# Performance work log

Measured on AMD Instinct MI355X. Metric: run time of the kernel, lower is better.

Reference implementation:

```python
import jax, jax.numpy as jnp
import numpy as np

N = 100_000
E = 1_600_000
D_IN, D_HID, D_OUT = 512, 256, 256


def setup_inputs() -> dict:
    key = jax.random.key(0)
    ks = jax.random.split(key, 10)
    x = jax.random.normal(ks[0], (N, D_IN), dtype=jnp.float32)
    edge_index = jax.random.randint(ks[1], (2, E), 0, N, dtype=jnp.int64)
    edge_weight = jax.random.uniform(ks[2], (E,), dtype=jnp.float32)
    # Glorot-ish init for the per-layer linear weights (PyG GCNConv: Linear w/o bias, bias added after aggregation)
    W1 = jax.random.normal(ks[3], (D_IN, D_HID), dtype=jnp.float32) * (1.0 / np.sqrt(D_IN))
    b1 = jnp.zeros((D_HID,), dtype=jnp.float32)
    W2 = jax.random.normal(ks[4], (D_HID, D_HID), dtype=jnp.float32) * (1.0 / np.sqrt(D_HID))
    b2 = jnp.zeros((D_HID,), dtype=jnp.float32)
    W3 = jax.random.normal(ks[5], (D_HID, D_OUT), dtype=jnp.float32) * (1.0 / np.sqrt(D_HID))
    b3 = jnp.zeros((D_OUT,), dtype=jnp.float32)
    return {"x": x, "edge_index": edge_index, "edge_weight": edge_weight,
            "W1": W1, "b1": b1, "W2": W2, "b2": b2, "W3": W3, "b3": b3}


def gcn_layer(h_in, W, b, row, col, ew, n):
    # PyG GCNConv with normalize=True, add_self_loops=True (fill value 1.0), aggr='add':
    # h = X W; deg[i] = sum of incoming edge weights (incl. self loop);
    # norm_e = deg^-1/2[row] * w_e * deg^-1/2[col]; out[col] += norm_e * h[row]; out += bias
    h = h_in @ W                                            # [n, d_out]
    deg = jnp.zeros((n,), h.dtype).at[col].add(ew) + 1.0    # +1 from self loop
    dinv = jnp.where(deg > 0, jax.lax.rsqrt(deg), 0.0)      # deg_inv_sqrt, inf -> 0
    norm = dinv[row] * ew * dinv[col]                       # [E]
    out = jnp.zeros_like(h).at[col].add(norm[:, None] * h[row])
    out = out + (dinv * dinv)[:, None] * h                  # self-loop contribution (norm_ii = dinv_i^2)
    return out + b


def reference(x, edge_index, edge_weight, W1, b1, W2, b2, W3, b3):
    row, col = edge_index[0], edge_index[1]
    n = x.shape[0]
    # dropout p=0.0 -> identity
    h = jax.nn.relu(gcn_layer(x, W1, b1, row, col, edge_weight, n))
    h = jax.nn.relu(gcn_layer(h, W2, b2, row, col, edge_weight, n))
    return gcn_layer(h, W3, b3, row, col, edge_weight, n)
```

## Files before the change

kernel.cpp:

```cpp
#include <hip/hip_runtime.h>
#include <hip/hip_bf16.h>


#define D 256
#define ELLW 48
#define BSH 7
#define NREP 8
#define RCAP 352
#define FIXSCALE 1099511627776.0f
#define FIXINV   9.094947017729282e-13

typedef unsigned short ushort_t;
typedef unsigned long long u64;
typedef float f32x4 __attribute__((ext_vector_type(4)));
typedef short bf16x8 __attribute__((ext_vector_type(8)));
typedef unsigned int u32x4 __attribute__((ext_vector_type(4)));
typedef unsigned int u32x8 __attribute__((ext_vector_type(8)));
typedef int i32x4 __attribute__((ext_vector_type(4)));

__device__ __forceinline__ float blo(unsigned u) { return __uint_as_float(u << 16); }
__device__ __forceinline__ float bhi(unsigned u) { return __uint_as_float(u & 0xFFFF0000u); }
__device__ __forceinline__ ushort_t f2b(float f) {
    unsigned u = __float_as_uint(f);
    return (ushort_t)((u + 0x7FFFu + ((u >> 16) & 1u)) >> 16);
}
__device__ __forceinline__ void gload_lds16(const ushort_t* g, ushort_t* l) {
    __builtin_amdgcn_global_load_lds((const __attribute__((address_space(1))) unsigned int*)g,
                                     (__attribute__((address_space(3))) unsigned int*)l, 16, 0, 0);
}

__global__ __launch_bounds__(256) void bin_p1(const int* __restrict__ row,
                                              const int* __restrict__ col,
                                              const float* __restrict__ ew,
                                              int* __restrict__ bfill,
                                              i32x4* __restrict__ bins, int E) {
    int e = blockIdx.x * 256 + threadIdx.x;
    int rep = blockIdx.x & (NREP - 1);
    if (e < E) {
        int c = __builtin_nontemporal_load(&col[e]);
        int r = __builtin_nontemporal_load(&row[e]);
        float w = __builtin_nontemporal_load(&ew[e]);
        int b = c >> BSH;
        int pos = atomicAdd(&bfill[(b * NREP + rep) * 16], 1);
        if (pos < RCAP) {
            i32x4 rec = {r, __float_as_int(w), c, 0};
            __builtin_nontemporal_store(rec, &bins[(size_t)b * (NREP * RCAP) + rep * RCAP + pos]);
        }
    }
}

__global__ __launch_bounds__(256) void bin_p2(const i32x4* __restrict__ bins,
                                              const int* __restrict__ bfill,
                                              int* __restrict__ cnt,
                                              float* __restrict__ dinv,
                                              u64* __restrict__ ell, int N) {
    __shared__ u64 sacc[1 << BSH];
    const int b = blockIdx.x;
    const int base = b << BSH;
    const int t = threadIdx.x;
    if (t < (1 << BSH)) sacc[t] = 0ull;
    __syncthreads();
#pragma unroll
    for (int rep = 0; rep < NREP; ++rep) {
        int fill = bfill[(b * NREP + rep) * 16];
        if (fill > RCAP) fill = RCAP;
        for (int i = t; i < fill; i += 256) {
            i32x4 rec = bins[(size_t)b * (NREP * RCAP) + rep * RCAP + i];
            int li = rec.z - base;
            float w = __int_as_float(rec.y);
            u64 pack = (1ull << 48) | (u64)(w * FIXSCALE);
            int pos = (int)(atomicAdd(&sacc[li], pack) >> 48);
            if (pos < ELLW)
                ell[(size_t)rec.z * ELLW + pos] = ((u64)(unsigned)rec.y << 32) | (unsigned)rec.x;
        }
    }
    __syncthreads();
    if (t < (1 << BSH)) {
        int node = base + t;
        if (node < N) {
            u64 p = sacc[t];
            int m = (int)(p >> 48);
            cnt[node] = (m > ELLW) ? ELLW : m;
            float sum = (float)((double)(p & 0xFFFFFFFFFFFFull) * FIXINV);
            dinv[node] = rsqrtf(sum + 1.0f);
        }
    }
}

__global__ __launch_bounds__(256) void sort_ell(const int* __restrict__ cnt,
                                                u64* __restrict__ ell, int N) {
    int node = blockIdx.x * 4 + (threadIdx.x >> 6);
    if (node >= N) return;
    int lane = threadIdx.x & 63;
    int m = cnt[node];
    if (m <= 1) return;
    unsigned key = (0x1FFFFu << 6) | lane;
    unsigned pw = 0;
    if (lane < m) {
        u64 r = ell[(size_t)node * ELLW + lane];
        key = (((unsigned)r) << 6) | lane;
        pw = (unsigned)(r >> 32);
    }
#pragma unroll
    for (int k = 2; k <= 64; k <<= 1) {
#pragma unroll
        for (int j = k >> 1; j > 0; j >>= 1) {
            unsigned pkey = __shfl_xor(key, j);
            unsigned ppw  = __shfl_xor(pw, j);
            bool dirUp = ((lane & k) == 0);
            bool lower = ((lane & j) == 0);
            bool takeOwn = ((key < pkey) == (lower == dirUp));
            key = takeOwn ? key : pkey;
            pw  = takeOwn ? pw  : ppw;
        }
    }
    if (lane < m)
        ell[(size_t)node * ELLW + lane] = (((u64)pw) << 32) | (key >> 6);
}

__global__ __launch_bounds__(256) void cvtT_kernel(const float* __restrict__ W,
                                                   ushort_t* __restrict__ WT, int K, int C) {
    int i = blockIdx.x * 256 + threadIdx.x;
    if (i < K * C) {
        int c = i / K, k = i - c * K;
        WT[i] = f2b(W[(size_t)k * C + c]);
    }
}

template <int K, bool AF32>
__global__ __launch_bounds__(256) void gemm_mfma(const void* __restrict__ Ap,
                                                 const ushort_t* __restrict__ WT,
                                                 ushort_t* __restrict__ C, int nvalid) {
    __shared__ ushort_t As[128 * 64];
    __shared__ ushort_t Bs[256 * 64];
    const int tid = threadIdx.x;
    const int lane = tid & 63, wave = tid >> 6;
    const int wrow = wave >> 1, wcol = wave & 1;
    const int fr = lane & 15, fq = lane >> 4;
    const int r0 = blockIdx.x * 128;

    f32x4 acc[4][8] = {};

    for (int k0 = 0; k0 < K; k0 += 64) {
        if constexpr (AF32) {
            const float* Af = (const float*)Ap;
#pragma unroll
            for (int i = 0; i < 8; ++i) {
                int idx = i * 256 + tid;
                int rowt = idx >> 4;
                int c4 = idx & 15;
                int grow = r0 + rowt;
                if (grow >= nvalid) grow = nvalid - 1;
                f32x4 v = __builtin_nontemporal_load(
                    (const f32x4*)&Af[(size_t)grow * K + k0 + c4 * 4]);
                __hip_bfloat162 b01 = __float22bfloat162_rn(make_float2(v[0], v[1]));
                __hip_bfloat162 b23 = __float22bfloat162_rn(make_float2(v[2], v[3]));
                uint2 st = make_uint2(*(unsigned*)&b01, *(unsigned*)&b23);
                int slot = c4 >> 1, half = c4 & 1;
                int off = rowt * 64 + ((slot ^ (rowt & 7)) << 3) + (half << 2);
                *(uint2*)&As[off] = st;
            }
        } else {
            const ushort_t* Ab = (const ushort_t*)Ap;
#pragma unroll
            for (int q = 0; q < 4; ++q) {
                int qa = wave * 4 + q;
                int rowt = qa * 8 + (lane >> 3);
                int g = (lane & 7) ^ (lane >> 3);
                gload_lds16(&Ab[(size_t)(r0 + rowt) * K + k0 + g * 8], &As[qa * 512]);
            }
        }
#pragma unroll
        for (int q = 0; q < 8; ++q) {
            int qb = wave * 8 + q;
            int rowt = qb * 8 + (lane >> 3);
            int g = (lane & 7) ^ (lane >> 3);
            gload_lds16(&WT[(size_t)rowt * K + k0 + g * 8], &Bs[qb * 512]);
        }
        __syncthreads();

#pragma unroll
        for (int kk = 0; kk < 2; ++kk) {
            int g = (kk * 4 + fq) ^ (fr & 7);
            bf16x8 aF[4];
#pragma unroll
            for (int m = 0; m < 4; ++m) {
                int arow = wrow * 64 + m * 16 + fr;
                aF[m] = *(const bf16x8*)&As[arow * 64 + g * 8];
            }
#pragma unroll
            for (int n = 0; n < 8; ++n) {
                int bcol = wcol * 128 + n * 16 + fr;
                bf16x8 bF = *(const bf16x8*)&Bs[bcol * 64 + g * 8];
#pragma unroll
                for (int m = 0; m < 4; ++m)
                    acc[m][n] = __builtin_amdgcn_mfma_f32_16x16x32_bf16(
                        bF, aF[m], acc[m][n], 0, 0, 0);
            }
        }
        __syncthreads();
    }

#pragma unroll
    for (int m = 0; m < 4; ++m) {
        int gr = r0 + wrow * 64 + m * 16 + fr;
        if (gr < nvalid) {
#pragma unroll
            for (int n = 0; n < 8; ++n) {
                ushort4 h;
                h.x = f2b(acc[m][n][0]); h.y = f2b(acc[m][n][1]);
                h.z = f2b(acc[m][n][2]); h.w = f2b(acc[m][n][3]);
                *(ushort4*)&C[(size_t)gr * D + wcol * 128 + n * 16 + fq * 4] = h;
            }
        }
    }
}

template <bool RELU, bool OUTF32>
__global__ __launch_bounds__(256) void agg_kernel(const ushort_t* __restrict__ hb,
                                                  const float* __restrict__ dinv,
                                                  const float* __restrict__ bias,
                                                  const int* __restrict__ cnt,
                                                  const u64* __restrict__ ell,
                                                  void* __restrict__ outp, int N) {
    int node = blockIdx.x * 4 + (threadIdx.x >> 6);
    if (node >= N) return;
    int lane = threadIdx.x & 63;
    int q = lane >> 4;
    int fl = lane & 15;
    float dn = dinv[node], d2 = dn * dn;

    u32x8 sv = *(const u32x8*)&hb[(size_t)node * 256 + fl * 16];
    float sc = (q == 0) ? d2 : 0.f;
    float a[16];
#pragma unroll
    for (int i = 0; i < 8; ++i) { a[2 * i] = sc * blo(sv[i]); a[2 * i + 1] = sc * bhi(sv[i]); }

    int m = cnt[node];
    int srcl = 0;
    float wl = 0.f;
    if (lane < m) {
        u64 r = ell[(size_t)node * ELLW + lane];
        srcl = (int)(unsigned)r;
        wl = dinv[srcl] * __uint_as_float((unsigned)(r >> 32)) * dn;
    }
    int steps = (m + 3) >> 2;
#pragma unroll 2
    for (int j = 0; j < steps; ++j) {
        int idx = 4 * j + q;
        int src = __shfl(srcl, idx);
        float w = __shfl(wl, idx);
        u32x8 v = *(const u32x8*)&hb[(size_t)src * 256 + fl * 16];
#pragma unroll
        for (int i = 0; i < 8; ++i) {
            a[2 * i]     = fmaf(w, blo(v[i]), a[2 * i]);
            a[2 * i + 1] = fmaf(w, bhi(v[i]), a[2 * i + 1]);
        }
    }
#pragma unroll
    for (int i = 0; i < 16; ++i) {
        a[i] += __shfl_xor(a[i], 16);
        a[i] += __shfl_xor(a[i], 32);
    }
    float r0, r1, r2, r3;
    if (q == 0)      { r0 = a[0];  r1 = a[1];  r2 = a[2];  r3 = a[3];  }
    else if (q == 1) { r0 = a[4];  r1 = a[5];  r2 = a[6];  r3 = a[7];  }
    else if (q == 2) { r0 = a[8];  r1 = a[9];  r2 = a[10]; r3 = a[11]; }
    else             { r0 = a[12]; r1 = a[13]; r2 = a[14]; r3 = a[15]; }
    f32x4 bb = *(const f32x4*)&bias[fl * 16 + q * 4];
    r0 += bb[0]; r1 += bb[1]; r2 += bb[2]; r3 += bb[3];
    if (RELU) {
        r0 = fmaxf(r0, 0.f); r1 = fmaxf(r1, 0.f);
        r2 = fmaxf(r2, 0.f); r3 = fmaxf(r3, 0.f);
    }
    if (OUTF32) {
        f32x4 o = {r0, r1, r2, r3};
        __builtin_nontemporal_store(
            o, (f32x4*)((float*)outp + (size_t)node * 256 + fl * 16 + q * 4));
    } else {
        u64 p = (u64)f2b(r0) | ((u64)f2b(r1) << 16) | ((u64)f2b(r2) << 32) | ((u64)f2b(r3) << 48);
        __builtin_nontemporal_store(
            p, (u64*)((ushort_t*)outp + (size_t)node * 256 + fl * 16 + q * 4));
    }
}

extern "C" void kernel_launch(void* const* d_in, const int* in_sizes, int n_in,
                              void* d_out, int out_size, void* d_ws, size_t ws_size,
                              hipStream_t stream) {
    const float* x  = (const float*)d_in[0];
    const int*   ei = (const int*)d_in[1];
    const float* ew = (const float*)d_in[2];
    const float* W1 = (const float*)d_in[3];
    const float* b1 = (const float*)d_in[4];
    const float* W2 = (const float*)d_in[5];
    const float* b2 = (const float*)d_in[6];
    const float* W3 = (const float*)d_in[7];
    const float* b3 = (const float*)d_in[8];
    const int N = in_sizes[0] / 512;
    const int E = in_sizes[2];
    const int* row = ei;
    const int* col = ei + E;
    float* out = (float*)d_out;

    const int MB = (N + 127) / 128;
    const size_t Npad = (size_t)MB * 128;
    const int NBU = (N + (1 << BSH) - 1) >> BSH;

    char* ws = (char*)d_ws;
    size_t off = 0;
    auto alloc = [&](size_t bytes) -> void* {
        void* p = ws + off;
        off += (bytes + 255) / 256 * 256;
        return p;
    };
    ushort_t* hb  = (ushort_t*)alloc(Npad * D * sizeof(ushort_t));
    u64*      ell = (u64*)alloc((size_t)N * ELLW * sizeof(u64));
    ushort_t* WT1 = (ushort_t*)alloc((size_t)512 * D * sizeof(ushort_t));
    ushort_t* WT2 = (ushort_t*)alloc((size_t)256 * D * sizeof(ushort_t));
    ushort_t* WT3 = (ushort_t*)alloc((size_t)256 * D * sizeof(ushort_t));
    int*   cnt    = (int*)alloc((size_t)N * sizeof(int));
    float* dinv   = (float*)alloc((size_t)N * sizeof(float));
    int*   bfill  = (int*)alloc((size_t)NBU * NREP * 16 * sizeof(int));
    i32x4* bins   = (i32x4*)hb;
    ushort_t* ab  = (ushort_t*)d_out;

    (void)hipMemsetAsync(bfill, 0, (size_t)NBU * NREP * 16 * sizeof(int), stream);

    int gE = (E + 255) / 256;
    int gA = (N + 3) / 4;
    cvtT_kernel<<<(512 * D + 255) / 256, 256, 0, stream>>>(W1, WT1, 512, D);
    cvtT_kernel<<<(256 * D + 255) / 256, 256, 0, stream>>>(W2, WT2, 256, D);
    cvtT_kernel<<<(256 * D + 255) / 256, 256, 0, stream>>>(W3, WT3, 256, D);
    bin_p1<<<gE, 256, 0, stream>>>(row, col, ew, bfill, bins, E);
    bin_p2<<<NBU, 256, 0, stream>>>(bins, bfill, cnt, dinv, ell, N);
    sort_ell<<<gA, 256, 0, stream>>>(cnt, ell, N);

    gemm_mfma<512, true><<<MB, 256, 0, stream>>>(x, WT1, hb, N);
    agg_kernel<true, false><<<gA, 256, 0, stream>>>(hb, dinv, b1, cnt, ell, ab, N);
    gemm_mfma<256, false><<<MB, 256, 0, stream>>>(ab, WT2, hb, N);
    agg_kernel<true, false><<<gA, 256, 0, stream>>>(hb, dinv, b2, cnt, ell, ab, N);
    gemm_mfma<256, false><<<MB, 256, 0, stream>>>(ab, WT3, hb, N);
    agg_kernel<false, true><<<gA, 256, 0, stream>>>(hb, dinv, b3, cnt, ell, out, N);
}
```

Measured before the change: 764.5 us.

## Replace per-node ELL gather with bucketed source-sorted LDS accumulation aggregation

Drops the ELL layout and the per-node bitonic sort. Edges are now counting-sorted within 64-node destination buckets by source-index range (four wave segments, each split into 32 source ranges). Aggregation runs one block per bucket and feature half: each of the four waves streams its segment's edges, gathers 128 features per source row, and accumulates into a shared-memory tile before the epilogue adds self-loop, bias and ReLU. The aim is better locality in the source gathers and no ELL width cap, at the cost of twice as many aggregation launches, serialized LDS read-modify-write per edge, and small gather transactions per edge.

```diff
diff --git a/kernel.cpp b/kernel.cpp
--- a/kernel.cpp
+++ b/kernel.cpp
@@ -3,19 +3,19 @@
 
 
 #define D 256
-#define ELLW 48
-#define BSH 7
+#define BSH 6
 #define NREP 8
-#define RCAP 352
+#define RCAP 224
+#define SCAP (NREP * RCAP)
 #define FIXSCALE 1099511627776.0f
 #define FIXINV   9.094947017729282e-13
 
 typedef unsigned short ushort_t;
 typedef unsigned long long u64;
+typedef float f32x2 __attribute__((ext_vector_type(2)));
 typedef float f32x4 __attribute__((ext_vector_type(4)));
 typedef short bf16x8 __attribute__((ext_vector_type(8)));
-typedef unsigned int u32x4 __attribute__((ext_vector_type(4)));
-typedef unsigned int u32x8 __attribute__((ext_vector_type(8)));
+typedef unsigned int u32x2 __attribute__((ext_vector_type(2)));
 typedef int i32x4 __attribute__((ext_vector_type(4)));
 
 __device__ __forceinline__ float blo(unsigned u) { return __uint_as_float(u << 16); }
@@ -49,73 +49,66 @@
     }
 }
 
-__global__ __launch_bounds__(256) void bin_p2(const i32x4* __restrict__ bins,
-                                              const int* __restrict__ bfill,
-                                              int* __restrict__ cnt,
-                                              float* __restrict__ dinv,
-                                              u64* __restrict__ ell, int N) {
-    __shared__ u64 sacc[1 << BSH];
-    const int b = blockIdx.x;
+__global__ __launch_bounds__(256) void bin_sort(const i32x4* __restrict__ bins,
+                                                const int* __restrict__ bfill,
+                                                float* __restrict__ dinv,
+                                                u64* __restrict__ srt,
+                                                int* __restrict__ segw, int N) {
+    __shared__ int scnt[128];
+    __shared__ int epre[128];
+    __shared__ u64 sacc[64];
+    const int b = blockIdx.x, t = threadIdx.x;
     const int base = b << BSH;
-    const int t = threadIdx.x;
-    if (t < (1 << BSH)) sacc[t] = 0ull;
-    __syncthreads();
-#pragma unroll
+    if (t < 128) scnt[t] = 0;
+    if (t < 64) sacc[t] = 0ull;
+    __syncthreads();
     for (int rep = 0; rep < NREP; ++rep) {
         int fill = bfill[(b * NREP + rep) * 16];
         if (fill > RCAP) fill = RCAP;
         for (int i = t; i < fill; i += 256) {
             i32x4 rec = bins[(size_t)b * (NREP * RCAP) + rep * RCAP + i];
-            int li = rec.z - base;
-            float w = __int_as_float(rec.y);
-            u64 pack = (1ull << 48) | (u64)(w * FIXSCALE);
-            int pos = (int)(atomicAdd(&sacc[li], pack) >> 48);
-            if (pos < ELLW)
-                ell[(size_t)rec.z * ELLW + pos] = ((u64)(unsigned)rec.y << 32) | (unsigned)rec.x;
-        }
-    }
-    __syncthreads();
-    if (t < (1 << BSH)) {
+            int dstl = rec.z & 63;
+            int key = ((dstl >> 4) << 5) | ((unsigned)rec.x >> 12);
+            atomicAdd(&scnt[key], 1);
+            atomicAdd(&sacc[dstl], (1ull << 48) | (u64)(__int_as_float(rec.y) * FIXSCALE));
+        }
+    }
+    __syncthreads();
+    int own = (t < 128) ? scnt[t] : 0;
+    if (t < 128) epre[t] = own;
+    __syncthreads();
+    for (int off = 1; off < 128; off <<= 1) {
+        int x = 0;
+        if (t < 128 && t >= off) x = epre[t - off];
+        __syncthreads();
+        if (t < 128) epre[t] += x;
+        __syncthreads();
+    }
+    int excl = (t < 128) ? (epre[t] - own) : 0;
+    if (t < 128 && (t & 31) == 0) segw[b * 5 + (t >> 5)] = excl;
+    if (t == 127) segw[b * 5 + 4] = epre[127];
+    __syncthreads();
+    if (t < 128) scnt[t] = excl;
+    __syncthreads();
+    for (int rep = 0; rep < NREP; ++rep) {
+        int fill = bfill[(b * NREP + rep) * 16];
+        if (fill > RCAP) fill = RCAP;
+        for (int i = t; i < fill; i += 256) {
+            i32x4 rec = bins[(size_t)b * (NREP * RCAP) + rep * RCAP + i];
+            int dstl = rec.z & 63;
+            int key = ((dstl >> 4) << 5) | ((unsigned)rec.x >> 12);
+            int pos = atomicAdd(&scnt[key], 1);
+            srt[(size_t)b * SCAP + pos] =
+                ((u64)(unsigned)rec.y << 32) | (unsigned)((rec.x << 6) | dstl);
+        }
+    }
+    if (t < 64) {
         int node = base + t;
         if (node < N) {
-            u64 p = sacc[t];
-            int m = (int)(p >> 48);
-            cnt[node] = (m > ELLW) ? ELLW : m;
-            float sum = (float)((double)(p & 0xFFFFFFFFFFFFull) * FIXINV);
+            float sum = (float)((double)(sacc[t] & 0xFFFFFFFFFFFFull) * FIXINV);
             dinv[node] = rsqrtf(sum + 1.0f);
         }
     }
-}
-
-__global__ __launch_bounds__(256) void sort_ell(const int* __restrict__ cnt,
-                                                u64* __restrict__ ell, int N) {
-    int node = blockIdx.x * 4 + (threadIdx.x >> 6);
-    if (node >= N) return;
-    int lane = threadIdx.x & 63;
-    int m = cnt[node];
-    if (m <= 1) return;
-    unsigned key = (0x1FFFFu << 6) | lane;
-    unsigned pw = 0;
-    if (lane < m) {
-        u64 r = ell[(size_t)node * ELLW + lane];
-        key = (((unsigned)r) << 6) | lane;
-        pw = (unsigned)(r >> 32);
-    }
-#pragma unroll
-    for (int k = 2; k <= 64; k <<= 1) {
-#pragma unroll
-        for (int j = k >> 1; j > 0; j >>= 1) {
-            unsigned pkey = __shfl_xor(key, j);
-            unsigned ppw  = __shfl_xor(pw, j);
-            bool dirUp = ((lane & k) == 0);
-            bool lower = ((lane & j) == 0);
-            bool takeOwn = ((key < pkey) == (lower == dirUp));
-            key = takeOwn ? key : pkey;
-            pw  = takeOwn ? pw  : ppw;
-        }
-    }
-    if (lane < m)
-        ell[(size_t)node * ELLW + lane] = (((u64)pw) << 32) | (key >> 6);
 }
 
 __global__ __launch_bounds__(256) void cvtT_kernel(const float* __restrict__ W,
@@ -217,70 +210,76 @@
 }
 
 template <bool RELU, bool OUTF32>
-__global__ __launch_bounds__(256) void agg_kernel(const ushort_t* __restrict__ hb,
+__global__ __launch_bounds__(256) void agg_bucket(const ushort_t* __restrict__ hb,
                                                   const float* __restrict__ dinv,
                                                   const float* __restrict__ bias,
-                                                  const int* __restrict__ cnt,
-                                                  const u64* __restrict__ ell,
-                                                  void* __restrict__ outp, int N) {
-    int node = blockIdx.x * 4 + (threadIdx.x >> 6);
-    if (node >= N) return;
-    int lane = threadIdx.x & 63;
-    int q = lane >> 4;
-    int fl = lane & 15;
-    float dn = dinv[node], d2 = dn * dn;
-
-    u32x8 sv = *(const u32x8*)&hb[(size_t)node * 256 + fl * 16];
-    float sc = (q == 0) ? d2 : 0.f;
-    float a[16];
-#pragma unroll
-    for (int i = 0; i < 8; ++i) { a[2 * i] = sc * blo(sv[i]); a[2 * i + 1] = sc * bhi(sv[i]); }
-
-    int m = cnt[node];
-    int srcl = 0;
-    float wl = 0.f;
-    if (lane < m) {
-        u64 r = ell[(size_t)node * ELLW + lane];
-        srcl = (int)(unsigned)r;
-        wl = dinv[srcl] * __uint_as_float((unsigned)(r >> 32)) * dn;
-    }
-    int steps = (m + 3) >> 2;
-#pragma unroll 2
-    for (int j = 0; j < steps; ++j) {
-        int idx = 4 * j + q;
-        int src = __shfl(srcl, idx);
-        float w = __shfl(wl, idx);
-        u32x8 v = *(const u32x8*)&hb[(size_t)src * 256 + fl * 16];
-#pragma unroll
-        for (int i = 0; i < 8; ++i) {
-            a[2 * i]     = fmaf(w, blo(v[i]), a[2 * i]);
-            a[2 * i + 1] = fmaf(w, bhi(v[i]), a[2 * i + 1]);
-        }
-    }
-#pragma unroll
-    for (int i = 0; i < 16; ++i) {
-        a[i] += __shfl_xor(a[i], 16);
-        a[i] += __shfl_xor(a[i], 32);
-    }
-    float r0, r1, r2, r3;
-    if (q == 0)      { r0 = a[0];  r1 = a[1];  r2 = a[2];  r3 = a[3];  }
-    else if (q == 1) { r0 = a[4];  r1 = a[5];  r2 = a[6];  r3 = a[7];  }
-    else if (q == 2) { r0 = a[8];  r1 = a[9];  r2 = a[10]; r3 = a[11]; }
-    else             { r0 = a[12]; r1 = a[13]; r2 = a[14]; r3 = a[15]; }
-    f32x4 bb = *(const f32x4*)&bias[fl * 16 + q * 4];
-    r0 += bb[0]; r1 += bb[1]; r2 += bb[2]; r3 += bb[3];
-    if (RELU) {
-        r0 = fmaxf(r0, 0.f); r1 = fmaxf(r1, 0.f);
-        r2 = fmaxf(r2, 0.f); r3 = fmaxf(r3, 0.f);
-    }
-    if (OUTF32) {
-        f32x4 o = {r0, r1, r2, r3};
-        __builtin_nontemporal_store(
-            o, (f32x4*)((float*)outp + (size_t)node * 256 + fl * 16 + q * 4));
-    } else {
-        u64 p = (u64)f2b(r0) | ((u64)f2b(r1) << 16) | ((u64)f2b(r2) << 32) | ((u64)f2b(r3) << 48);
-        __builtin_nontemporal_store(
-            p, (u64*)((ushort_t*)outp + (size_t)node * 256 + fl * 16 + q * 4));
+                                                  const u64* __restrict__ srt,
+                                                  const int* __restrict__ segw,
+                                                  void* __restrict__ outp, int N, int half) {
+    __shared__ float acc[64 * 128];
+    __shared__ float sdinv[64];
+    const int b = blockIdx.x, t = threadIdx.x;
+    const int w = t >> 6, lane = t & 63;
+    const int base = b << BSH;
+    const int fb = half * 128;
+
+    if (t < 64) {
+        int node = base + t;
+        sdinv[t] = (node < N) ? dinv[node] : 0.f;
+    }
+#pragma unroll
+    for (int k = 0; k < 8; ++k)
+        *(f32x4*)&acc[(k * 256 + t) * 4] = (f32x4){0.f, 0.f, 0.f, 0.f};
+    __syncthreads();
+
+    const int s0 = segw[b * 5 + w];
+    const int s1 = segw[b * 5 + w + 1];
+    const u64* sb = &srt[(size_t)b * SCAP];
+
+    for (int i0 = s0; i0 < s1; i0 += 64) {
+        int nb = s1 - i0;
+        if (nb > 64) nb = 64;
+        u64 rv = (i0 + lane < s1) ? sb[i0 + lane] : 0ull;
+        unsigned klo_all = (unsigned)rv;
+        unsigned whi_all = (unsigned)(rv >> 32);
+        float nrm_all = dinv[klo_all >> 6] * __uint_as_float(whi_all) * sdinv[klo_all & 63];
+#pragma unroll 4
+        for (int j = 0; j < nb; ++j) {
+            unsigned klo = __shfl(klo_all, j);
+            float nrm = __shfl(nrm_all, j);
+            int src = klo >> 6, dstl = klo & 63;
+            unsigned v = *(const unsigned*)&hb[(size_t)src * 256 + fb + lane * 2];
+            float* ap = &acc[dstl * 128 + lane * 2];
+            f32x2 a = *(f32x2*)ap;
+            a[0] = fmaf(nrm, blo(v), a[0]);
+            a[1] = fmaf(nrm, bhi(v), a[1]);
+            *(f32x2*)ap = a;
+        }
+    }
+    __syncthreads();
+
+    const f32x2 bb = *(const f32x2*)&bias[fb + lane * 2];
+#pragma unroll 4
+    for (int it = 0; it < 16; ++it) {
+        int nl = w * 16 + it;
+        int node = base + nl;
+        if (node < N) {
+            float dn = sdinv[nl], d2 = dn * dn;
+            unsigned sv = *(const unsigned*)&hb[(size_t)node * 256 + fb + lane * 2];
+            f32x2 a = *(const f32x2*)&acc[nl * 128 + lane * 2];
+            float r0 = fmaf(d2, blo(sv), a[0]) + bb[0];
+            float r1 = fmaf(d2, bhi(sv), a[1]) + bb[1];
+            if (RELU) { r0 = fmaxf(r0, 0.f); r1 = fmaxf(r1, 0.f); }
+            if (OUTF32) {
+                f32x2 o = {r0, r1};
+                __builtin_nontemporal_store(
+                    o, (f32x2*)((float*)outp + (size_t)node * 256 + fb + lane * 2));
+            } else {
+                unsigned p = (unsigned)f2b(r0) | ((unsigned)f2b(r1) << 16);
+                __builtin_nontemporal_store(
+                    p, (unsigned*)((ushort_t*)outp + (size_t)node * 256 + fb + lane * 2));
+            }
+        }
     }
 }
 
@@ -314,31 +313,32 @@
         return p;
     };
     ushort_t* hb  = (ushort_t*)alloc(Npad * D * sizeof(ushort_t));
-    u64*      ell = (u64*)alloc((size_t)N * ELLW * sizeof(u64));
+    u64*      srt = (u64*)alloc((size_t)NBU * SCAP * sizeof(u64));
     ushort_t* WT1 = (ushort_t*)alloc((size_t)512 * D * sizeof(ushort_t));
     ushort_t* WT2 = (ushort_t*)alloc((size_t)256 * D * sizeof(ushort_t));
     ushort_t* WT3 = (ushort_t*)alloc((size_t)256 * D * sizeof(ushort_t));
-    int*   cnt    = (int*)alloc((size_t)N * sizeof(int));
     float* dinv   = (float*)alloc((size_t)N * sizeof(float));
     int*   bfill  = (int*)alloc((size_t)NBU * NREP * 16 * sizeof(int));
+    int*   segw   = (int*)alloc((size_t)NBU * 5 * sizeof(int));
     i32x4* bins   = (i32x4*)hb;
     ushort_t* ab  = (ushort_t*)d_out;
 
     (void)hipMemsetAsync(bfill, 0, (size_t)NBU * NREP * 16 * sizeof(int), stream);
 
     int gE = (E + 255) / 256;
-    int gA = (N + 3) / 4;
     cvtT_kernel<<<(512 * D + 255) / 256, 256, 0, stream>>>(W1, WT1, 512, D);
     cvtT_kernel<<<(256 * D + 255) / 256, 256, 0, stream>>>(W2, WT2, 256, D);
     cvtT_kernel<<<(256 * D + 255) / 256, 256, 0, stream>>>(W3, WT3, 256, D);
     bin_p1<<<gE, 256, 0, stream>>>(row, col, ew, bfill, bins, E);
-    bin_p2<<<NBU, 256, 0, stream>>>(bins, bfill, cnt, dinv, ell, N);
-    sort_ell<<<gA, 256, 0, stream>>>(cnt, ell, N);
+    bin_sort<<<NBU, 256, 0, stream>>>(bins, bfill, dinv, srt, segw, N);
 
     gemm_mfma<512, true><<<MB, 256, 0, stream>>>(x, WT1, hb, N);
-    agg_kernel<true, false><<<gA, 256, 0, stream>>>(hb, dinv, b1, cnt, ell, ab, N);
+    agg_bucket<true, false><<<NBU, 256, 0, stream>>>(hb, dinv, b1, srt, segw, ab, N, 0);
+    agg_bucket<true, false><<<NBU, 256, 0, stream>>>(hb, dinv, b1, srt, segw, ab, N, 1);
     gemm_mfma<256, false><<<MB, 256, 0, stream>>>(ab, WT2, hb, N);
-    agg_kernel<true, false><<<gA, 256, 0, stream>>>(hb, dinv, b2, cnt, ell, ab, N);
+    agg_bucket<true, false><<<NBU, 256, 0, stream>>>(hb, dinv, b2, srt, segw, ab, N, 0);
+    agg_bucket<true, false><<<NBU, 256, 0, stream>>>(hb, dinv, b2, srt, segw, ab, N, 1);
     gemm_mfma<256, false><<<MB, 256, 0, stream>>>(ab, WT3, hb, N);
-    agg_kernel<false, true><<<gA, 256, 0, stream>>>(hb, dinv, b3, cnt, ell, out, N);
-}
+    agg_bucket<false, true><<<NBU, 256, 0, stream>>>(hb, dinv, b3, srt, segw, out, N, 0);
+    agg_bucket<false, true><<<NBU, 256, 0, stream>>>(hb, dinv, b3, srt, segw, out, N, 1);
+}
```

Measured after the change: 1.527 ms. 2x slower.

## Split aggregation into two feature-half passes and drop ELL neighbor sort

Applied to the files above, without the earlier changes.

Each aggregation is split into two launches, each covering 128 of the 256 features. Each pass gathers 16-byte rows instead of 32-byte ones, so the gathered working set is halved per pass and is meant to fit better in cache. The sort_ell kernel, which ordered neighbors by source index, is removed, and the ELL loads become nontemporal. The cost is twice the ELL and index reads, extra launches, and loss of the source-ordered gather locality the sort provided.

```diff
diff --git a/kernel.cpp b/kernel.cpp
--- a/kernel.cpp
+++ b/kernel.cpp
@@ -12,10 +12,10 @@
 
 typedef unsigned short ushort_t;
 typedef unsigned long long u64;
+typedef float f32x2 __attribute__((ext_vector_type(2)));
 typedef float f32x4 __attribute__((ext_vector_type(4)));
 typedef short bf16x8 __attribute__((ext_vector_type(8)));
 typedef unsigned int u32x4 __attribute__((ext_vector_type(4)));
-typedef unsigned int u32x8 __attribute__((ext_vector_type(8)));
 typedef int i32x4 __attribute__((ext_vector_type(4)));
 
 __device__ __forceinline__ float blo(unsigned u) { return __uint_as_float(u << 16); }
@@ -87,37 +87,6 @@
     }
 }
 
-__global__ __launch_bounds__(256) void sort_ell(const int* __restrict__ cnt,
-                                                u64* __restrict__ ell, int N) {
-    int node = blockIdx.x * 4 + (threadIdx.x >> 6);
-    if (node >= N) return;
-    int lane = threadIdx.x & 63;
-    int m = cnt[node];
-    if (m <= 1) return;
-    unsigned key = (0x1FFFFu << 6) | lane;
-    unsigned pw = 0;
-    if (lane < m) {
-        u64 r = ell[(size_t)node * ELLW + lane];
-        key = (((unsigned)r) << 6) | lane;
-        pw = (unsigned)(r >> 32);
-    }
-#pragma unroll
-    for (int k = 2; k <= 64; k <<= 1) {
-#pragma unroll
-        for (int j = k >> 1; j > 0; j >>= 1) {
-            unsigned pkey = __shfl_xor(key, j);
-            unsigned ppw  = __shfl_xor(pw, j);
-            bool dirUp = ((lane & k) == 0);
-            bool lower = ((lane & j) == 0);
-            bool takeOwn = ((key < pkey) == (lower == dirUp));
-            key = takeOwn ? key : pkey;
-            pw  = takeOwn ? pw  : ppw;
-        }
-    }
-    if (lane < m)
-        ell[(size_t)node * ELLW + lane] = (((u64)pw) << 32) | (key >> 6);
-}
-
 __global__ __launch_bounds__(256) void cvtT_kernel(const float* __restrict__ W,
                                                    ushort_t* __restrict__ WT, int K, int C) {
     int i = blockIdx.x * 256 + threadIdx.x;
@@ -217,12 +186,12 @@
 }
 
 template <bool RELU, bool OUTF32>
-__global__ __launch_bounds__(256) void agg_kernel(const ushort_t* __restrict__ hb,
-                                                  const float* __restrict__ dinv,
-                                                  const float* __restrict__ bias,
-                                                  const int* __restrict__ cnt,
-                                                  const u64* __restrict__ ell,
-                                                  void* __restrict__ outp, int N) {
+__global__ __launch_bounds__(256) void agg_half(const ushort_t* __restrict__ hb,
+                                                const float* __restrict__ dinv,
+                                                const float* __restrict__ bias,
+                                                const int* __restrict__ cnt,
+                                                const u64* __restrict__ ell,
+                                                void* __restrict__ outp, int N, int fb) {
     int node = blockIdx.x * 4 + (threadIdx.x >> 6);
     if (node >= N) return;
     int lane = threadIdx.x & 63;
@@ -230,17 +199,17 @@
     int fl = lane & 15;
     float dn = dinv[node], d2 = dn * dn;
 
-    u32x8 sv = *(const u32x8*)&hb[(size_t)node * 256 + fl * 16];
+    u32x4 sv = *(const u32x4*)&hb[(size_t)node * 256 + fb + fl * 8];
     float sc = (q == 0) ? d2 : 0.f;
-    float a[16];
-#pragma unroll
-    for (int i = 0; i < 8; ++i) { a[2 * i] = sc * blo(sv[i]); a[2 * i + 1] = sc * bhi(sv[i]); }
+    float a[8];
+#pragma unroll
+    for (int i = 0; i < 4; ++i) { a[2 * i] = sc * blo(sv[i]); a[2 * i + 1] = sc * bhi(sv[i]); }
 
     int m = cnt[node];
     int srcl = 0;
     float wl = 0.f;
     if (lane < m) {
-        u64 r = ell[(size_t)node * ELLW + lane];
+        u64 r = __builtin_nontemporal_load(&ell[(size_t)node * ELLW + lane]);
         srcl = (int)(unsigned)r;
         wl = dinv[srcl] * __uint_as_float((unsigned)(r >> 32)) * dn;
     }
@@ -250,37 +219,33 @@
         int idx = 4 * j + q;
         int src = __shfl(srcl, idx);
         float w = __shfl(wl, idx);
-        u32x8 v = *(const u32x8*)&hb[(size_t)src * 256 + fl * 16];
-#pragma unroll
-        for (int i = 0; i < 8; ++i) {
+        u32x4 v = *(const u32x4*)&hb[(size_t)src * 256 + fb + fl * 8];
+#pragma unroll
+        for (int i = 0; i < 4; ++i) {
             a[2 * i]     = fmaf(w, blo(v[i]), a[2 * i]);
             a[2 * i + 1] = fmaf(w, bhi(v[i]), a[2 * i + 1]);
         }
     }
 #pragma unroll
-    for (int i = 0; i < 16; ++i) {
+    for (int i = 0; i < 8; ++i) {
         a[i] += __shfl_xor(a[i], 16);
         a[i] += __shfl_xor(a[i], 32);
     }
-    float r0, r1, r2, r3;
-    if (q == 0)      { r0 = a[0];  r1 = a[1];  r2 = a[2];  r3 = a[3];  }
-    else if (q == 1) { r0 = a[4];  r1 = a[5];  r2 = a[6];  r3 = a[7];  }
-    else if (q == 2) { r0 = a[8];  r1 = a[9];  r2 = a[10]; r3 = a[11]; }
-    else             { r0 = a[12]; r1 = a[13]; r2 = a[14]; r3 = a[15]; }
-    f32x4 bb = *(const f32x4*)&bias[fl * 16 + q * 4];
-    r0 += bb[0]; r1 += bb[1]; r2 += bb[2]; r3 += bb[3];
-    if (RELU) {
-        r0 = fmaxf(r0, 0.f); r1 = fmaxf(r1, 0.f);
-        r2 = fmaxf(r2, 0.f); r3 = fmaxf(r3, 0.f);
-    }
+    float r0, r1;
+    if (q == 0)      { r0 = a[0]; r1 = a[1]; }
+    else if (q == 1) { r0 = a[2]; r1 = a[3]; }
+    else if (q == 2) { r0 = a[4]; r1 = a[5]; }
+    else             { r0 = a[6]; r1 = a[7]; }
+    int feat = fb + fl * 8 + q * 2;
+    f32x2 bb = *(const f32x2*)&bias[feat];
+    r0 += bb[0]; r1 += bb[1];
+    if (RELU) { r0 = fmaxf(r0, 0.f); r1 = fmaxf(r1, 0.f); }
     if (OUTF32) {
-        f32x4 o = {r0, r1, r2, r3};
-        __builtin_nontemporal_store(
-            o, (f32x4*)((float*)outp + (size_t)node * 256 + fl * 16 + q * 4));
+        f32x2 o = {r0, r1};
+        __builtin_nontemporal_store(o, (f32x2*)((float*)outp + (size_t)node * 256 + feat));
     } else {
-        u64 p = (u64)f2b(r0) | ((u64)f2b(r1) << 16) | ((u64)f2b(r2) << 32) | ((u64)f2b(r3) << 48);
-        __builtin_nontemporal_store(
-            p, (u64*)((ushort_t*)outp + (size_t)node * 256 + fl * 16 + q * 4));
+        unsigned p = (unsigned)f2b(r0) | ((unsigned)f2b(r1) << 16);
+        __builtin_nontemporal_store(p, (unsigned*)((ushort_t*)outp + (size_t)node * 256 + feat));
     }
 }
 
@@ -333,12 +298,14 @@
     cvtT_kernel<<<(256 * D + 255) / 256, 256, 0, stream>>>(W3, WT3, 256, D);
     bin_p1<<<gE, 256, 0, stream>>>(row, col, ew, bfill, bins, E);
     bin_p2<<<NBU, 256, 0, stream>>>(bins, bfill, cnt, dinv, ell, N);
-    sort_ell<<<gA, 256, 0, stream>>>(cnt, ell, N);
 
     gemm_mfma<512, true><<<MB, 256, 0, stream>>>(x, WT1, hb, N);
-    agg_kernel<true, false><<<gA, 256, 0, stream>>>(hb, dinv, b1, cnt, ell, ab, N);
+    agg_half<true, false><<<gA, 256, 0, stream>>>(hb, dinv, b1, cnt, ell, ab, N, 0);
+    agg_half<true, false><<<gA, 256, 0, stream>>>(hb, dinv, b1, cnt, ell, ab, N, 128);
     gemm_mfma<256, false><<<MB, 256, 0, stream>>>(ab, WT2, hb, N);
-    agg_kernel<true, false><<<gA, 256, 0, stream>>>(hb, dinv, b2, cnt, ell, ab, N);
+    agg_half<true, false><<<gA, 256, 0, stream>>>(hb, dinv, b2, cnt, ell, ab, N, 0);
+    agg_half<true, false><<<gA, 256, 0, stream>>>(hb, dinv, b2, cnt, ell, ab, N, 128);
     gemm_mfma<256, false><<<MB, 256, 0, stream>>>(ab, WT3, hb, N);
-    agg_kernel<false, true><<<gA, 256, 0, stream>>>(hb, dinv, b3, cnt, ell, out, N);
-}
+    agg_half<false, true><<<gA, 256, 0, stream>>>(hb, dinv, b3, cnt, ell, out, N, 0);
+    agg_half<false, true><<<gA, 256, 0, stream>>>(hb, dinv, b3, cnt, ell, out, N, 128);
+}
```

Measured after the change: 753.7 us. Within noise of the previous version (-1.4%).
